# Kernel optimization log

Measured on AMD Instinct MI355X. Metric: run time of the kernel, lower is better.

The kernel has to match this reference:

```python
import jax, jax.numpy as jnp
import numpy as np

N, C, K, H = 131072, 512, 128, 8  # points, channels, patch_size, heads


def setup_inputs() -> dict:
    key = jax.random.key(0)
    ks = jax.random.split(key, 6)
    feat = jax.random.normal(ks[0], (N, C), dtype=jnp.float32)
    Wqkv = jax.random.normal(ks[1], (C, 3 * C), dtype=jnp.float32) * 0.02
    bqkv = jax.random.normal(ks[2], (3 * C,), dtype=jnp.float32) * 0.02
    Wproj = jax.random.normal(ks[3], (C, C), dtype=jnp.float32) * 0.02
    bproj = jax.random.normal(ks[4], (C,), dtype=jnp.float32) * 0.02
    order = jax.random.permutation(ks[5], N).astype(jnp.int64)  # serialized order (all clusters full)
    inverse = jnp.argsort(order).astype(jnp.int64)              # serialized inverse
    return {"feat": feat, "Wqkv": Wqkv, "bqkv": bqkv, "Wproj": Wproj,
            "bproj": bproj, "order": order, "inverse": inverse}


def reference(feat, Wqkv, bqkv, Wproj, bproj, order, inverse):
    hd = C // H
    scale = hd ** -0.5
    qkv = feat @ Wqkv + bqkv                 # [N, 3C]
    qkv = qkv[order]                         # gather by serialized order
    qkv = qkv.reshape(-1, K, 3, H, hd)       # [W, K, 3, H, hd]
    qkv = jnp.moveaxis(qkv, 2, 0)            # [3, W, K, H, hd]
    q = jnp.swapaxes(qkv[0], 1, 2)           # [W, H, K, hd]
    k = jnp.swapaxes(qkv[1], 1, 2)
    v = jnp.swapaxes(qkv[2], 1, 2)
    # upcast_attention / upcast_softmax -> compute scores & softmax in fp32
    attn = jnp.einsum('whkd,whjd->whkj', (q * scale).astype(jnp.float32),
                      k.astype(jnp.float32))             # [W, H, K, K]
    attn = jax.nn.softmax(attn, axis=-1).astype(feat.dtype)
    out = jnp.einsum('whkj,whjd->whkd', attn, v)          # [W, H, K, hd]
    out = jnp.swapaxes(out, 1, 2).reshape(-1, C)          # [N, C]
    out = out[inverse]                                    # scatter back via inverse
    out = out @ Wproj + bproj
    return out
```

## Files before the change

kernel.cpp:

```cpp
#include <hip/hip_runtime.h>
#include <hip/hip_bf16.h>
#include <cstdint>
#include <cstddef>

typedef __bf16 bf16;
typedef __bf16 bf16x8 __attribute__((ext_vector_type(8)));
typedef float f32x4 __attribute__((ext_vector_type(4)));

#define N_PTS 131072
#define CDIM  512
#define C3    1536
#define HD    64
#define NH    8
#define KWIN  128

static __device__ __forceinline__ bf16 cvt(float x) { return (bf16)x; }

static __device__ __forceinline__ void gld16(const bf16* g, bf16* l) {
    __builtin_amdgcn_global_load_lds(
        (const __attribute__((address_space(1))) void*)g,
        (__attribute__((address_space(3))) void*)l, 16, 0, 0);
}

__global__ __launch_bounds__(256) void k_prep(
    const float* __restrict__ Wqkv, const float* __restrict__ Wproj,
    bf16* __restrict__ Wqkv_t, bf16* __restrict__ Wproj_t)
{
    int idx = blockIdx.x * 256 + threadIdx.x;
    if (idx < CDIM * C3) {
        int k = idx / C3, c = idx % C3;
        Wqkv_t[(size_t)c * CDIM + k] = cvt(Wqkv[idx]);
    } else {
        int j = idx - CDIM * C3;
        if (j < CDIM * CDIM) {
            int k = j / CDIM, c = j % CDIM;
            Wproj_t[(size_t)c * CDIM + k] = cvt(Wproj[j]);
        }
    }
}

__global__ __launch_bounds__(256) void k_gather(
    const float* __restrict__ feat, const int* __restrict__ order,
    bf16* __restrict__ feat_g)
{
    int row = blockIdx.x * 2 + (threadIdx.x >> 7);
    int c   = (threadIdx.x & 127) << 2;
    int src = order[row];
    float4 v = *reinterpret_cast<const float4*>(feat + (size_t)src * CDIM + c);
    union { bf16 e[4]; uint2 u; } pk;
    pk.e[0] = cvt(v.x); pk.e[1] = cvt(v.y); pk.e[2] = cvt(v.z); pk.e[3] = cvt(v.w);
    *reinterpret_cast<uint2*>(feat_g + (size_t)row * CDIM + c) = pk.u;
}

template <bool F32OUT, int NT>
__global__ __launch_bounds__(256) void k_gemm(
    const bf16* __restrict__ Ag, const bf16* __restrict__ Bt,
    const float* __restrict__ bias, void* __restrict__ outp)
{
    __shared__ __align__(16) bf16 As[128 * 64];
    __shared__ __align__(16) bf16 Bs[128 * 64];

    const int t    = threadIdx.x;
    const int lane = t & 63;
    const int wv   = t >> 6;
    const int wr   = wv >> 1, wc = wv & 1;
    const int g    = lane >> 4, r16 = lane & 15;

    const int nwg = gridDim.x;
    const int bid = blockIdx.x;
    const int swz = (bid & 7) * (nwg >> 3) + (bid >> 3);
    const int m0  = (swz / NT) * 128;
    const int n0  = (swz % NT) * 128;

    int c_lin[4], srow[4], scol[4];
#pragma unroll
    for (int j = 0; j < 4; ++j) {
        c_lin[j] = (wv * 4 + j) * 64 + lane;
        int c_src = c_lin[j] ^ ((c_lin[j] >> 3) & 7);
        srow[j] = c_src >> 3;
        scol[j] = (c_src & 7) << 3;
    }

    f32x4 acc[4][4];
    const f32x4 z = {0.f, 0.f, 0.f, 0.f};
#pragma unroll
    for (int m = 0; m < 4; ++m)
#pragma unroll
        for (int n = 0; n < 4; ++n) acc[m][n] = z;

    for (int k0 = 0; k0 < CDIM; k0 += 64) {
#pragma unroll
        for (int j = 0; j < 4; ++j) {
            gld16(Ag + (size_t)(m0 + srow[j]) * CDIM + k0 + scol[j],
                  &As[(wv * 4 + j) * 512]);
            gld16(Bt + (size_t)(n0 + srow[j]) * CDIM + k0 + scol[j],
                  &Bs[(wv * 4 + j) * 512]);
        }
        __syncthreads();

        bf16x8 af[4][2], bfv[4][2];
#pragma unroll
        for (int m = 0; m < 4; ++m) {
            int row = wr * 64 + m * 16 + r16;
#pragma unroll
            for (int kk = 0; kk < 2; ++kk) {
                int boff = row * 128 + ((kk * 64 + g * 16) ^ ((row & 7) << 4));
                af[m][kk] = *reinterpret_cast<const bf16x8*>(
                    reinterpret_cast<const char*>(As) + boff);
            }
        }
#pragma unroll
        for (int n = 0; n < 4; ++n) {
            int row = wc * 64 + n * 16 + r16;
#pragma unroll
            for (int kk = 0; kk < 2; ++kk) {
                int boff = row * 128 + ((kk * 64 + g * 16) ^ ((row & 7) << 4));
                bfv[n][kk] = *reinterpret_cast<const bf16x8*>(
                    reinterpret_cast<const char*>(Bs) + boff);
            }
        }
#pragma unroll
        for (int kk = 0; kk < 2; ++kk)
#pragma unroll
            for (int m = 0; m < 4; ++m)
#pragma unroll
                for (int n = 0; n < 4; ++n)
                    acc[m][n] = __builtin_amdgcn_mfma_f32_16x16x32_bf16(
                        af[m][kk], bfv[n][kk], acc[m][n], 0, 0, 0);
        __syncthreads();
    }

    const int ldo = NT * 128;
#pragma unroll
    for (int n = 0; n < 4; ++n) {
        int col = n0 + wc * 64 + n * 16 + r16;
        float b = bias[col];
#pragma unroll
        for (int m = 0; m < 4; ++m)
#pragma unroll
            for (int j = 0; j < 4; ++j) {
                int row = m0 + wr * 64 + m * 16 + g * 4 + j;
                if (F32OUT)
                    reinterpret_cast<float*>(outp)[(size_t)row * ldo + col] =
                        acc[m][n][j] + b;
                else
                    reinterpret_cast<bf16*>(outp)[(size_t)row * ldo + col] =
                        cvt(acc[m][n][j] + b);
            }
    }
}

__global__ __launch_bounds__(256) void k_attn(
    const bf16* __restrict__ qkv_s, const int* __restrict__ order,
    bf16* __restrict__ attn_g)
{
    __shared__ __align__(16) char smem[36864 + 64 * 136 * 2];
    __shared__ int ord_s[KWIN];
    bf16 (*Q)[72]   = reinterpret_cast<bf16 (*)[72]>(smem);
    bf16 (*Kt)[72]  = reinterpret_cast<bf16 (*)[72]>(smem + 128 * 72 * 2);
    bf16 (*P)[136]  = reinterpret_cast<bf16 (*)[136]>(smem);
    bf16 (*Vt)[136] = reinterpret_cast<bf16 (*)[136]>(smem + 36864);

    const int t    = threadIdx.x;
    const int lane = t & 63;
    const int wv   = t >> 6;
    const int g    = lane >> 4, r16 = lane & 15;
    const int h    = blockIdx.x;
    const int w    = blockIdx.y;

    const bf16* base = qkv_s + (size_t)w * KWIN * C3 + h * HD;

    if (t < KWIN) ord_s[t] = order[w * KWIN + t];

#pragma unroll
    for (int it = 0; it < 4; ++it) {
        int s   = it * 256 + t;
        int tok = s >> 3;
        int c8  = (s & 7) << 3;
        size_t roff = (size_t)tok * C3 + c8;
        *reinterpret_cast<uint4*>(&Q[tok][c8])  =
            *reinterpret_cast<const uint4*>(base + roff);
        *reinterpret_cast<uint4*>(&Kt[tok][c8]) =
            *reinterpret_cast<const uint4*>(base + roff + CDIM);
        uint4 vvec = *reinterpret_cast<const uint4*>(base + roff + 2 * CDIM);
        const bf16* ve = reinterpret_cast<const bf16*>(&vvec);
#pragma unroll
        for (int i = 0; i < 8; ++i) Vt[c8 + i][tok] = ve[i];
    }
    __syncthreads();

    f32x4 sc[2][8];
    const f32x4 z = {0.f, 0.f, 0.f, 0.f};
#pragma unroll
    for (int m = 0; m < 2; ++m)
#pragma unroll
        for (int n = 0; n < 8; ++n) sc[m][n] = z;

#pragma unroll
    for (int ks = 0; ks < 2; ++ks) {
        bf16x8 aq[2];
#pragma unroll
        for (int m = 0; m < 2; ++m)
            aq[m] = *reinterpret_cast<const bf16x8*>(
                &Q[wv * 32 + m * 16 + r16][ks * 32 + g * 8]);
#pragma unroll
        for (int n = 0; n < 8; ++n) {
            bf16x8 bk = *reinterpret_cast<const bf16x8*>(
                &Kt[n * 16 + r16][ks * 32 + g * 8]);
#pragma unroll
            for (int m = 0; m < 2; ++m)
                sc[m][n] = __builtin_amdgcn_mfma_f32_16x16x32_bf16(
                    aq[m], bk, sc[m][n], 0, 0, 0);
        }
    }

    const float scale = 0.125f;
    float inv_sum[2][4];
#pragma unroll
    for (int m = 0; m < 2; ++m) {
#pragma unroll
        for (int j = 0; j < 4; ++j) {
            float mx = -3.0e38f;
#pragma unroll
            for (int n = 0; n < 8; ++n) mx = fmaxf(mx, sc[m][n][j]);
            mx = fmaxf(mx, __shfl_xor(mx, 1));
            mx = fmaxf(mx, __shfl_xor(mx, 2));
            mx = fmaxf(mx, __shfl_xor(mx, 4));
            mx = fmaxf(mx, __shfl_xor(mx, 8));
            mx *= scale;
            float ssum = 0.f;
#pragma unroll
            for (int n = 0; n < 8; ++n) {
                float p = __expf(sc[m][n][j] * scale - mx);
                sc[m][n][j] = p;
                ssum += p;
            }
            ssum += __shfl_xor(ssum, 1);
            ssum += __shfl_xor(ssum, 2);
            ssum += __shfl_xor(ssum, 4);
            ssum += __shfl_xor(ssum, 8);
            inv_sum[m][j] = 1.f / ssum;
        }
    }

    __syncthreads();

#pragma unroll
    for (int m = 0; m < 2; ++m)
#pragma unroll
        for (int n = 0; n < 8; ++n)
#pragma unroll
            for (int j = 0; j < 4; ++j)
                P[wv * 32 + m * 16 + g * 4 + j][n * 16 + r16] =
                    cvt(sc[m][n][j] * inv_sum[m][j]);

    f32x4 o[2][4];
#pragma unroll
    for (int m = 0; m < 2; ++m)
#pragma unroll
        for (int n = 0; n < 4; ++n) o[m][n] = z;

#pragma unroll
    for (int kt = 0; kt < 4; ++kt) {
        bf16x8 ap[2];
#pragma unroll
        for (int m = 0; m < 2; ++m)
            ap[m] = *reinterpret_cast<const bf16x8*>(
                &P[wv * 32 + m * 16 + r16][kt * 32 + g * 8]);
#pragma unroll
        for (int n = 0; n < 4; ++n) {
            bf16x8 bv = *reinterpret_cast<const bf16x8*>(
                &Vt[n * 16 + r16][kt * 32 + g * 8]);
#pragma unroll
            for (int m = 0; m < 2; ++m)
                o[m][n] = __builtin_amdgcn_mfma_f32_16x16x32_bf16(
                    ap[m], bv, o[m][n], 0, 0, 0);
        }
    }

#pragma unroll
    for (int m = 0; m < 2; ++m)
#pragma unroll
        for (int n = 0; n < 4; ++n)
#pragma unroll
            for (int j = 0; j < 4; ++j) {
                int tok  = wv * 32 + m * 16 + g * 4 + j;
                int d    = n * 16 + r16;
                int drow = ord_s[tok];
                attn_g[(size_t)drow * CDIM + h * HD + d] = cvt(o[m][n][j]);
            }
}

extern "C" void kernel_launch(void* const* d_in, const int* in_sizes, int n_in,
                              void* d_out, int out_size, void* d_ws, size_t ws_size,
                              hipStream_t stream)
{
    const float* feat    = (const float*)d_in[0];
    const float* Wqkv    = (const float*)d_in[1];
    const float* bqkv    = (const float*)d_in[2];
    const float* Wproj   = (const float*)d_in[3];
    const float* bproj   = (const float*)d_in[4];
    const int*   order   = (const int*)d_in[5];
    float* out = (float*)d_out;

    const size_t qkv_bytes  = (size_t)N_PTS * C3 * sizeof(bf16);
    const size_t gat_bytes  = (size_t)N_PTS * CDIM * sizeof(bf16);
    const size_t wq_bytes   = (size_t)C3 * CDIM * sizeof(bf16);
    const size_t wp_bytes   = (size_t)CDIM * CDIM * sizeof(bf16);
    if (ws_size < qkv_bytes + gat_bytes + wq_bytes + wp_bytes) return;

    bf16* qkv_s   = (bf16*)d_ws;
    bf16* shared134 = (bf16*)((char*)d_ws + qkv_bytes);
    bf16* Wqkv_t  = (bf16*)((char*)d_ws + qkv_bytes + gat_bytes);
    bf16* Wproj_t = (bf16*)((char*)d_ws + qkv_bytes + gat_bytes + wq_bytes);

    k_prep<<<dim3((CDIM * C3 + CDIM * CDIM + 255) / 256), 256, 0, stream>>>(
        Wqkv, Wproj, Wqkv_t, Wproj_t);
    k_gather<<<dim3(N_PTS / 2), 256, 0, stream>>>(feat, order, shared134);
    k_gemm<false, C3 / 128><<<dim3((N_PTS / 128) * (C3 / 128)), 256, 0, stream>>>(
        shared134, Wqkv_t, bqkv, qkv_s);
    k_attn<<<dim3(NH, N_PTS / KWIN), 256, 0, stream>>>(qkv_s, order, shared134);
    k_gemm<true, CDIM / 128><<<dim3((N_PTS / 128) * (CDIM / 128)), 256, 0, stream>>>(
        shared134, Wproj_t, bproj, out);
}
```

Measured before the change: 700.8 us.

## Rewrite GEMM as 256x256 tiles with four-stage async LDS pipeline

Both projection GEMMs now use 512-thread blocks computing 256x256 output tiles, each wave owning 128x64. A four-buffer ring of direct global-to-LDS loads with K-step 32 is kept three stages ahead, synchronised by explicit vmcnt waits and barriers. MFMA sections are raised in priority with s_setprio. This is meant to overlap memory latency with compute and increase operand reuse per LDS byte. The cost is heavier register use (32 accumulators per thread), fewer blocks, and the removal of the XOR swizzle, which may reintroduce LDS bank conflicts.

```diff
diff --git a/kernel.cpp b/kernel.cpp
--- a/kernel.cpp
+++ b/kernel.cpp
@@ -53,99 +53,123 @@
 }
 
 template <bool F32OUT, int NT>
-__global__ __launch_bounds__(256) void k_gemm(
+__global__ __launch_bounds__(512) void k_gemm(
     const bf16* __restrict__ Ag, const bf16* __restrict__ Bt,
     const float* __restrict__ bias, void* __restrict__ outp)
 {
-    __shared__ __align__(16) bf16 As[128 * 64];
-    __shared__ __align__(16) bf16 Bs[128 * 64];
+    __shared__ __align__(16) bf16 As[4][256 * 32];
+    __shared__ __align__(16) bf16 Bs[4][256 * 32];
 
     const int t    = threadIdx.x;
     const int lane = t & 63;
     const int wv   = t >> 6;
-    const int wr   = wv >> 1, wc = wv & 1;
+    const int wr   = wv >> 2;
+    const int wc   = wv & 3;
     const int g    = lane >> 4, r16 = lane & 15;
 
     const int nwg = gridDim.x;
     const int bid = blockIdx.x;
     const int swz = (bid & 7) * (nwg >> 3) + (bid >> 3);
-    const int m0  = (swz / NT) * 128;
-    const int n0  = (swz % NT) * 128;
-
-    int c_lin[4], srow[4], scol[4];
-#pragma unroll
-    for (int j = 0; j < 4; ++j) {
-        c_lin[j] = (wv * 4 + j) * 64 + lane;
-        int c_src = c_lin[j] ^ ((c_lin[j] >> 3) & 7);
-        srow[j] = c_src >> 3;
-        scol[j] = (c_src & 7) << 3;
-    }
-
-    f32x4 acc[4][4];
+    const int m0  = (swz / NT) * 256;
+    const int n0  = (swz % NT) * 256;
+
+    const int L0 = wv * 64 + lane;
+    const int L1 = L0 + 512;
+    const bf16* sA0 = Ag + (size_t)(m0 + (L0 >> 2)) * CDIM + (L0 & 3) * 8;
+    const bf16* sA1 = Ag + (size_t)(m0 + (L1 >> 2)) * CDIM + (L1 & 3) * 8;
+    const bf16* sB0 = Bt + (size_t)(n0 + (L0 >> 2)) * CDIM + (L0 & 3) * 8;
+    const bf16* sB1 = Bt + (size_t)(n0 + (L1 >> 2)) * CDIM + (L1 & 3) * 8;
+
+    int aoff[8], boff[4];
+#pragma unroll
+    for (int i = 0; i < 8; ++i) {
+        int row = wr * 128 + i * 16 + r16;
+        aoff[i] = row * 64 + g * 16;
+    }
+#pragma unroll
+    for (int n = 0; n < 4; ++n) {
+        int row = wc * 64 + n * 16 + r16;
+        boff[n] = row * 64 + g * 16;
+    }
+
+    f32x4 acc[8][4];
     const f32x4 z = {0.f, 0.f, 0.f, 0.f};
 #pragma unroll
-    for (int m = 0; m < 4; ++m)
-#pragma unroll
-        for (int n = 0; n < 4; ++n) acc[m][n] = z;
-
-    for (int k0 = 0; k0 < CDIM; k0 += 64) {
-#pragma unroll
-        for (int j = 0; j < 4; ++j) {
-            gld16(Ag + (size_t)(m0 + srow[j]) * CDIM + k0 + scol[j],
-                  &As[(wv * 4 + j) * 512]);
-            gld16(Bt + (size_t)(n0 + srow[j]) * CDIM + k0 + scol[j],
-                  &Bs[(wv * 4 + j) * 512]);
-        }
-        __syncthreads();
-
-        bf16x8 af[4][2], bfv[4][2];
-#pragma unroll
-        for (int m = 0; m < 4; ++m) {
-            int row = wr * 64 + m * 16 + r16;
-#pragma unroll
-            for (int kk = 0; kk < 2; ++kk) {
-                int boff = row * 128 + ((kk * 64 + g * 16) ^ ((row & 7) << 4));
-                af[m][kk] = *reinterpret_cast<const bf16x8*>(
-                    reinterpret_cast<const char*>(As) + boff);
-            }
-        }
-#pragma unroll
-        for (int n = 0; n < 4; ++n) {
-            int row = wc * 64 + n * 16 + r16;
-#pragma unroll
-            for (int kk = 0; kk < 2; ++kk) {
-                int boff = row * 128 + ((kk * 64 + g * 16) ^ ((row & 7) << 4));
-                bfv[n][kk] = *reinterpret_cast<const bf16x8*>(
-                    reinterpret_cast<const char*>(Bs) + boff);
-            }
-        }
-#pragma unroll
-        for (int kk = 0; kk < 2; ++kk)
-#pragma unroll
-            for (int m = 0; m < 4; ++m)
-#pragma unroll
-                for (int n = 0; n < 4; ++n)
-                    acc[m][n] = __builtin_amdgcn_mfma_f32_16x16x32_bf16(
-                        af[m][kk], bfv[n][kk], acc[m][n], 0, 0, 0);
-        __syncthreads();
-    }
-
-    const int ldo = NT * 128;
+    for (int i = 0; i < 8; ++i)
+#pragma unroll
+        for (int n = 0; n < 4; ++n) acc[i][n] = z;
+
+    auto stage = [&](int kt) {
+        const int b  = kt & 3;
+        const int ko = kt * 32;
+        gld16(sA0 + ko, &As[b][(size_t)wv * 64 * 8]);
+        gld16(sA1 + ko, &As[b][(size_t)(512 + wv * 64) * 8]);
+        gld16(sB0 + ko, &Bs[b][(size_t)wv * 64 * 8]);
+        gld16(sB1 + ko, &Bs[b][(size_t)(512 + wv * 64) * 8]);
+    };
+
+    auto compute = [&](int kt) {
+        const int b = kt & 3;
+        bf16x8 af[8], bv[4];
+#pragma unroll
+        for (int i = 0; i < 8; ++i)
+            af[i] = *reinterpret_cast<const bf16x8*>(
+                reinterpret_cast<const char*>(&As[b][0]) + aoff[i]);
+#pragma unroll
+        for (int n = 0; n < 4; ++n)
+            bv[n] = *reinterpret_cast<const bf16x8*>(
+                reinterpret_cast<const char*>(&Bs[b][0]) + boff[n]);
+        asm volatile("s_waitcnt lgkmcnt(0)" ::: "memory");
+        __builtin_amdgcn_sched_barrier(0);
+        __builtin_amdgcn_s_setprio(1);
+#pragma unroll
+        for (int i = 0; i < 8; ++i)
+#pragma unroll
+            for (int n = 0; n < 4; ++n)
+                acc[i][n] = __builtin_amdgcn_mfma_f32_16x16x32_bf16(
+                    af[i], bv[n], acc[i][n], 0, 0, 0);
+        __builtin_amdgcn_s_setprio(0);
+    };
+
+    stage(0); stage(1); stage(2);
+    asm volatile("s_waitcnt vmcnt(8)" ::: "memory");
+    __builtin_amdgcn_s_barrier();
+    __builtin_amdgcn_sched_barrier(0);
+
+#pragma unroll
+    for (int kt = 0; kt < 13; ++kt) {
+        stage(kt + 3);
+        compute(kt);
+        asm volatile("s_waitcnt vmcnt(8)" ::: "memory");
+        __builtin_amdgcn_s_barrier();
+        __builtin_amdgcn_sched_barrier(0);
+    }
+    compute(13);
+    asm volatile("s_waitcnt vmcnt(4)" ::: "memory");
+    __builtin_amdgcn_s_barrier();
+    __builtin_amdgcn_sched_barrier(0);
+    compute(14);
+    asm volatile("s_waitcnt vmcnt(0)" ::: "memory");
+    __builtin_amdgcn_s_barrier();
+    __builtin_amdgcn_sched_barrier(0);
+    compute(15);
+
+    const int ldo = NT * 256;
 #pragma unroll
     for (int n = 0; n < 4; ++n) {
         int col = n0 + wc * 64 + n * 16 + r16;
         float b = bias[col];
 #pragma unroll
-        for (int m = 0; m < 4; ++m)
+        for (int i = 0; i < 8; ++i)
 #pragma unroll
             for (int j = 0; j < 4; ++j) {
-                int row = m0 + wr * 64 + m * 16 + g * 4 + j;
+                int row = m0 + wr * 128 + i * 16 + g * 4 + j;
                 if (F32OUT)
                     reinterpret_cast<float*>(outp)[(size_t)row * ldo + col] =
-                        acc[m][n][j] + b;
+                        acc[i][n][j] + b;
                 else
                     reinterpret_cast<bf16*>(outp)[(size_t)row * ldo + col] =
-                        cvt(acc[m][n][j] + b);
+                        cvt(acc[i][n][j] + b);
             }
     }
 }
@@ -309,17 +333,17 @@
     const size_t wp_bytes   = (size_t)CDIM * CDIM * sizeof(bf16);
     if (ws_size < qkv_bytes + gat_bytes + wq_bytes + wp_bytes) return;
 
-    bf16* qkv_s   = (bf16*)d_ws;
+    bf16* qkv_s     = (bf16*)d_ws;
     bf16* shared134 = (bf16*)((char*)d_ws + qkv_bytes);
-    bf16* Wqkv_t  = (bf16*)((char*)d_ws + qkv_bytes + gat_bytes);
-    bf16* Wproj_t = (bf16*)((char*)d_ws + qkv_bytes + gat_bytes + wq_bytes);
+    bf16* Wqkv_t    = (bf16*)((char*)d_ws + qkv_bytes + gat_bytes);
+    bf16* Wproj_t   = (bf16*)((char*)d_ws + qkv_bytes + gat_bytes + wq_bytes);
 
     k_prep<<<dim3((CDIM * C3 + CDIM * CDIM + 255) / 256), 256, 0, stream>>>(
         Wqkv, Wproj, Wqkv_t, Wproj_t);
     k_gather<<<dim3(N_PTS / 2), 256, 0, stream>>>(feat, order, shared134);
-    k_gemm<false, C3 / 128><<<dim3((N_PTS / 128) * (C3 / 128)), 256, 0, stream>>>(
+    k_gemm<false, C3 / 256><<<dim3((N_PTS / 256) * (C3 / 256)), 512, 0, stream>>>(
         shared134, Wqkv_t, bqkv, qkv_s);
     k_attn<<<dim3(NH, N_PTS / KWIN), 256, 0, stream>>>(qkv_s, order, shared134);
-    k_gemm<true, CDIM / 128><<<dim3((N_PTS / 128) * (CDIM / 128)), 256, 0, stream>>>(
+    k_gemm<true, CDIM / 256><<<dim3((N_PTS / 256) * (CDIM / 256)), 512, 0, stream>>>(
         shared134, Wproj_t, bproj, out);
 }
```

After: 664.8 us. 5.1% less time.
